# Kernel tuning notes

Hardware: AMD Instinct MI355X
Metric: run time of the kernel (lower is better)

The kernel has to match this reference:

```python
import jax, jax.numpy as jnp
import numpy as np
from jax import lax

B, C, H, W = 32, 128, 56, 56
SIZE = C * H * W
EPS = 1e-5
SLOPE = 0.1


def setup_inputs() -> dict:
    key = jax.random.key(0)
    ks = jax.random.split(key, 12)
    return {
        "ax": jax.random.normal(ks[0], (B, C, H, W), dtype=jnp.float32),
        "mx": jax.random.normal(ks[1], (B, C, H, W), dtype=jnp.float32),
        # grouped conv1d (groups=SIZE, k=2, no bias) == per-position pair weights [SIZE, 2]
        "cfc_w": jax.random.normal(ks[2], (SIZE, 2), dtype=jnp.float32) * 0.1,
        # BatchNorm1d (eval mode) params over SIZE channels
        "bn_gamma": jax.random.normal(ks[3], (SIZE,), dtype=jnp.float32) * 0.1 + 1.0,
        "bn_beta": jax.random.normal(ks[4], (SIZE,), dtype=jnp.float32) * 0.1,
        "bn_mean": jax.random.normal(ks[5], (SIZE,), dtype=jnp.float32) * 0.1,
        "bn_var": jax.random.uniform(ks[6], (SIZE,), dtype=jnp.float32, minval=0.5, maxval=1.5),
        # conv3x3, C->C, bias
        "conv_w": jax.random.normal(ks[7], (C, C, 3, 3), dtype=jnp.float32) * (1.0 / np.sqrt(C * 9)),
        "conv_b": jax.random.normal(ks[8], (C,), dtype=jnp.float32) * 0.01,
        # BatchNorm2d (eval mode) params over C channels
        "bn2_gamma": jax.random.normal(ks[9], (C,), dtype=jnp.float32) * 0.1 + 1.0,
        "bn2_beta": jax.random.normal(ks[10], (C,), dtype=jnp.float32) * 0.1,
        "bn2_mean": jax.random.normal(ks[11], (C,), dtype=jnp.float32) * 0.1,
        "bn2_var": jax.random.uniform(jax.random.fold_in(key, 99), (C,), dtype=jnp.float32, minval=0.5, maxval=1.5),
    }


def reference(ax, mx, cfc_w, bn_gamma, bn_beta, bn_mean, bn_var,
              conv_w, conv_b, bn2_gamma, bn2_beta, bn2_mean, bn2_var):
    b, c, h, w = ax.shape
    a = ax.reshape(b, -1)  # [B, SIZE]
    m = mx.reshape(b, -1)
    # degenerate grouped Conv1d(k=2, groups=SIZE): z_i = w_i0 * a_i + w_i1 * m_i
    z = cfc_w[:, 0] * a + cfc_w[:, 1] * m
    # BatchNorm1d (eval) + LeakyReLU(0.1)
    z = (z - bn_mean) * (bn_gamma / jnp.sqrt(bn_var + EPS)) + bn_beta
    z = jax.nn.leaky_relu(z, SLOPE).reshape(b, c, h, w)
    # conv3x3 (stride 1, pad 1) + bias
    y = lax.conv_general_dilated(z, conv_w, window_strides=(1, 1),
                                 padding=((1, 1), (1, 1)),
                                 dimension_numbers=("NCHW", "OIHW", "NCHW"))
    y = y + conv_b[None, :, None, None]
    # BatchNorm2d (eval) + LeakyReLU(0.1)
    scale = (bn2_gamma / jnp.sqrt(bn2_var + EPS))[None, :, None, None]
    y = (y - bn2_mean[None, :, None, None]) * scale + bn2_beta[None, :, None, None]
    return jax.nn.leaky_relu(y, SLOPE)
```

## Files before the change

kernel.cpp:

```cpp
#include <hip/hip_runtime.h>

#define B_ 32
#define C_ 128
#define H_ 56
#define W_ 56
#define HW_ (H_*W_)
#define SIZE_ (C_*HW_)
#define NPIX_ (B_*HW_)
#define HP_ 58
#define WP_ 58
#define PLANE_ (HP_*WP_*C_)
#define K_ 1152
#define EPS_ 1e-5f
#define SLOPE_ 0.1f

typedef __bf16 bf16x8 __attribute__((ext_vector_type(8)));
typedef float  f32x4  __attribute__((ext_vector_type(4)));

__device__ __forceinline__ ushort f2bf(float x) {
    union { float f; unsigned u; } v; v.f = x;
    return (ushort)((v.u + 0x7FFFu + ((v.u >> 16) & 1u)) >> 16);
}
__device__ __forceinline__ float lrelu(float z) { return z > 0.f ? z : SLOPE_ * z; }

__device__ __forceinline__ void glds16(const ushort* g, ushort* l) {
    __builtin_amdgcn_global_load_lds(
        (const __attribute__((address_space(1))) unsigned int*)g,
        (__attribute__((address_space(3))) unsigned int*)l, 16, 0, 0);
}

__global__ __launch_bounds__(256) void prep_kernel(
    const float* __restrict__ conv_w, const float* __restrict__ conv_b,
    const float* __restrict__ g2, const float* __restrict__ b2,
    const float* __restrict__ m2, const float* __restrict__ v2,
    const float2* __restrict__ cfc, const float* __restrict__ g1,
    const float* __restrict__ b1, const float* __restrict__ mu1,
    const float* __restrict__ v1,
    ushort* __restrict__ wA, float* __restrict__ scale2, float* __restrict__ shift2,
    float* __restrict__ p0, float* __restrict__ p1, float* __restrict__ p2)
{
    int tid = blockIdx.x * 256 + threadIdx.x;
    if (tid < C_ * K_) {
        int co = tid / K_;
        int k  = tid - co * K_;
        int khkw = k >> 7, ci = k & 127;
        int kh = khkw / 3, kw = khkw - 3 * kh;
        wA[tid] = f2bf(conv_w[((co * C_ + ci) * 3 + kh) * 3 + kw]);
    }
    if (tid < C_) {
        float sc = g2[tid] * rsqrtf(v2[tid] + EPS_);
        scale2[tid] = sc;
        shift2[tid] = (conv_b[tid] - m2[tid]) * sc + b2[tid];
    }
    if (tid < SIZE_) {
        float sc = g1[tid] * rsqrtf(v1[tid] + EPS_);
        float2 wv = cfc[tid];
        p0[tid] = wv.x * sc;
        p1[tid] = wv.y * sc;
        p2[tid] = b1[tid] - mu1[tid] * sc;
    }
}

__global__ __launch_bounds__(256) void zfuse_kernel(
    const float4* __restrict__ ax, const float4* __restrict__ mx,
    const float4* __restrict__ p0, const float4* __restrict__ p1,
    const float4* __restrict__ p2, ushort* __restrict__ zp)
{
    __shared__ ushort tile[W_ * 132];
    const int hp = blockIdx.x, b = blockIdx.y;
    const int tid = threadIdx.x;
    ushort* row = zp + (size_t)b * PLANE_ + (size_t)hp * (WP_ * C_);
    if (hp == 0 || hp == HP_ - 1) {
        uint2* r2 = (uint2*)row;
        for (int i = tid; i < WP_ * C_ / 4; i += 256) r2[i] = make_uint2(0u, 0u);
        return;
    }
    const int h = hp - 1;
    const int base4 = (b * SIZE_) >> 2;
    for (int i = tid; i < 1792; i += 256) {
        int c  = i / 14;
        int w4 = i - c * 14;
        int s4 = c * (HW_ / 4) + h * (W_ / 4) + w4;
        float4 a = ax[base4 + s4];
        float4 m = mx[base4 + s4];
        float4 q0 = p0[s4], q1 = p1[s4], q2 = p2[s4];
        int wb = w4 * 4;
        tile[(wb + 0) * 132 + c] = f2bf(lrelu(a.x * q0.x + m.x * q1.x + q2.x));
        tile[(wb + 1) * 132 + c] = f2bf(lrelu(a.y * q0.y + m.y * q1.y + q2.y));
        tile[(wb + 2) * 132 + c] = f2bf(lrelu(a.z * q0.z + m.z * q1.z + q2.z));
        tile[(wb + 3) * 132 + c] = f2bf(lrelu(a.w * q0.w + m.w * q1.w + q2.w));
    }
    __syncthreads();
    if (tid < C_) {
        row[tid] = 0;
        row[(WP_ - 1) * C_ + tid] = 0;
    }
    for (int j = tid; j < 1792; j += 256) {
        int w = j >> 5, cc = j & 31;
        *(uint2*)(row + C_ + w * C_ + cc * 4) = *(const uint2*)(tile + w * 132 + cc * 4);
    }
}

__global__ __launch_bounds__(256) void conv_kernel(
    const ushort* __restrict__ zp, const ushort* __restrict__ wA,
    const float* __restrict__ scale2, const float* __restrict__ shift2,
    float* __restrict__ out)
{
    __shared__ ushort As[2][128 * 32];
    __shared__ ushort Bs[2][128 * 32];

    const int tid  = threadIdx.x;
    const int wave = tid >> 6, lane = tid & 63;
    const int l16  = lane & 15, quad = lane >> 4;
    const int pbase = blockIdx.x * 128;

    const int srow = wave * 32 + (lane >> 2);
    const int skey = (srow >> 1) & 3;
    const int sch  = (lane & 3) ^ skey;
    const ushort* agA = wA + srow * K_ + sch * 8;

    int pf0 = pbase + srow;
    int bb0 = pf0 / HW_, pi0 = pf0 - bb0 * HW_;
    int h0 = pi0 / W_, w0 = pi0 - h0 * W_;
    const ushort* bgB0 = zp + (size_t)bb0 * PLANE_ + (h0 * WP_ + w0) * C_ + sch * 8;
    int pf1 = pf0 + 16;
    int bb1 = pf1 / HW_, pi1 = pf1 - bb1 * HW_;
    int h1 = pi1 / W_, w1 = pi1 - h1 * W_;
    const ushort* bgB1 = zp + (size_t)bb1 * PLANE_ + (h1 * WP_ + w1) * C_ + sch * 8;

    const int lofs0 = (wave * 32) * 32;
    const int lofs1 = (wave * 32 + 16) * 32;

    const int cob = (wave & 1) * 64;
    const int pxb = (wave >> 1) * 64;
    const int rquad = quad ^ ((l16 >> 1) & 3);

    f32x4 acc[4][4] = {};

#define STAGE(buf, aoff, boff)                                    \
    do {                                                          \
        glds16(agA + (aoff),           As[buf] + lofs0);          \
        glds16(agA + 16 * K_ + (aoff), As[buf] + lofs1);          \
        glds16(bgB0 + (boff),          Bs[buf] + lofs0);          \
        glds16(bgB1 + (boff),          Bs[buf] + lofs1);          \
    } while (0)

    STAGE(0, 0, 0);
    __syncthreads();

    int zoff = 0, kw = 0;
    for (int tap = 0; tap < 9; ++tap) {
        const int znext = (kw == 2) ? zoff + (WP_ - 2) * C_ : zoff + C_;
        #pragma unroll
        for (int ks = 0; ks < 4; ++ks) {
            const int buf  = ks & 1;
            const int step = tap * 4 + ks;
            if (step < 35) {
                const int boffn = (ks < 3) ? zoff + (ks + 1) * 32 : znext;
                STAGE(buf ^ 1, (step + 1) * 32, boffn);
            }
            bf16x8 af[4], bfr[4];
            #pragma unroll
            for (int mt = 0; mt < 4; ++mt)
                af[mt] = *(const bf16x8*)(As[buf] + (cob + mt * 16 + l16) * 32 + rquad * 8);
            #pragma unroll
            for (int nt = 0; nt < 4; ++nt)
                bfr[nt] = *(const bf16x8*)(Bs[buf] + (pxb + nt * 16 + l16) * 32 + rquad * 8);
            #pragma unroll
            for (int mt = 0; mt < 4; ++mt)
                #pragma unroll
                for (int nt = 0; nt < 4; ++nt)
                    acc[mt][nt] = __builtin_amdgcn_mfma_f32_16x16x32_bf16(
                        af[mt], bfr[nt], acc[mt][nt], 0, 0, 0);
            __syncthreads();
        }
        zoff = znext;
        if (kw == 2) kw = 0; else ++kw;
    }
#undef STAGE

    int pob[4];
    #pragma unroll
    for (int nt = 0; nt < 4; ++nt) {
        int pf = pbase + pxb + nt * 16 + l16;
        int bb = pf / HW_;
        pob[nt] = bb * SIZE_ + (pf - bb * HW_);
    }
    #pragma unroll
    for (int mt = 0; mt < 4; ++mt) {
        #pragma unroll
        for (int r = 0; r < 4; ++r) {
            int co = cob + mt * 16 + quad * 4 + r;
            float sc = scale2[co], sh = shift2[co];
            #pragma unroll
            for (int nt = 0; nt < 4; ++nt) {
                float v = acc[mt][nt][r] * sc + sh;
                out[(size_t)pob[nt] + co * HW_] = lrelu(v);
            }
        }
    }
}

extern "C" void kernel_launch(void* const* d_in, const int* in_sizes, int n_in,
                              void* d_out, int out_size, void* d_ws, size_t ws_size,
                              hipStream_t stream) {
    const float* ax     = (const float*)d_in[0];
    const float* mx     = (const float*)d_in[1];
    const float* cfc    = (const float*)d_in[2];
    const float* bn_g   = (const float*)d_in[3];
    const float* bn_b   = (const float*)d_in[4];
    const float* bn_m   = (const float*)d_in[5];
    const float* bn_v   = (const float*)d_in[6];
    const float* conv_w = (const float*)d_in[7];
    const float* conv_b = (const float*)d_in[8];
    const float* g2     = (const float*)d_in[9];
    const float* b2     = (const float*)d_in[10];
    const float* m2     = (const float*)d_in[11];
    const float* v2     = (const float*)d_in[12];
    float* out = (float*)d_out;

    char* ws = (char*)d_ws;
    ushort* zp     = (ushort*)ws;
    ushort* wA     = (ushort*)(ws + 27557888);
    float*  scale2 = (float*)(ws + 27852800);
    float*  shift2 = (float*)(ws + 27853312);
    float*  p0     = (float*)(ws + 27853824);
    float*  p1     = (float*)(ws + 29459456);
    float*  p2     = (float*)(ws + 31065088);

    prep_kernel<<<dim3((SIZE_ + 255) / 256), 256, 0, stream>>>(
        conv_w, conv_b, g2, b2, m2, v2, (const float2*)cfc,
        bn_g, bn_b, bn_m, bn_v, wA, scale2, shift2, p0, p1, p2);
    zfuse_kernel<<<dim3(HP_, B_), 256, 0, stream>>>(
        (const float4*)ax, (const float4*)mx,
        (const float4*)p0, (const float4*)p1, (const float4*)p2, zp);
    conv_kernel<<<dim3(NPIX_ / 128), 256, 0, stream>>>(zp, wA, scale2, shift2, out);
}
```

Before: 237.3 us.

## Triple-buffer conv K-loop with explicit vmcnt waits and single barrier

Replaces the double-buffered LDS pipeline in the conv GEMM with a three-stage ring. Loads are issued two steps ahead, and the wait uses s_waitcnt vmcnt(4) plus one barrier per step instead of a full sync after the MFMAs. The 36-step loop is fully unrolled with compile-time B offsets, and launch bounds now ask for 3 blocks per CU. The goal is to hide global-to-LDS latency behind MFMA work, at the cost of 50% more LDS and a tighter register budget.

New measurement: 241.8 us. Within noise of the previous version (+1.9%).

```diff
diff --git a/kernel.cpp b/kernel.cpp
--- a/kernel.cpp
+++ b/kernel.cpp
@@ -101,13 +101,13 @@
     }
 }
 
-__global__ __launch_bounds__(256) void conv_kernel(
+__global__ __launch_bounds__(256, 3) void conv_kernel(
     const ushort* __restrict__ zp, const ushort* __restrict__ wA,
     const float* __restrict__ scale2, const float* __restrict__ shift2,
     float* __restrict__ out)
 {
-    __shared__ ushort As[2][128 * 32];
-    __shared__ ushort Bs[2][128 * 32];
+    __shared__ ushort As[3][128 * 32];
+    __shared__ ushort Bs[3][128 * 32];
 
     const int tid  = threadIdx.x;
     const int wave = tid >> 6, lane = tid & 63;
@@ -145,39 +145,38 @@
         glds16(bgB1 + (boff),          Bs[buf] + lofs1);          \
     } while (0)
 
-    STAGE(0, 0, 0);
-    __syncthreads();
-
-    int zoff = 0, kw = 0;
-    for (int tap = 0; tap < 9; ++tap) {
-        const int znext = (kw == 2) ? zoff + (WP_ - 2) * C_ : zoff + C_;
-        #pragma unroll
-        for (int ks = 0; ks < 4; ++ks) {
-            const int buf  = ks & 1;
-            const int step = tap * 4 + ks;
-            if (step < 35) {
-                const int boffn = (ks < 3) ? zoff + (ks + 1) * 32 : znext;
-                STAGE(buf ^ 1, (step + 1) * 32, boffn);
-            }
-            bf16x8 af[4], bfr[4];
-            #pragma unroll
-            for (int mt = 0; mt < 4; ++mt)
-                af[mt] = *(const bf16x8*)(As[buf] + (cob + mt * 16 + l16) * 32 + rquad * 8);
+#define BOFF(t) ((((t) >> 2) / 3 * WP_ + ((t) >> 2) % 3) * C_ + ((t) & 3) * 32)
+
+    STAGE(0, 0, BOFF(0));
+    STAGE(1, 32, BOFF(1));
+
+    #pragma unroll
+    for (int t = 0; t < 36; ++t) {
+        if (t < 35) asm volatile("s_waitcnt vmcnt(4)" ::: "memory");
+        else        asm volatile("s_waitcnt vmcnt(0)" ::: "memory");
+        __builtin_amdgcn_s_barrier();
+        __builtin_amdgcn_sched_barrier(0);
+        if (t <= 33) {
+            const int t2 = t + 2;
+            STAGE(t2 % 3, t2 * 32, BOFF(t2));
+        }
+        const int buf = t % 3;
+        bf16x8 af[4], bfr[4];
+        #pragma unroll
+        for (int mt = 0; mt < 4; ++mt)
+            af[mt] = *(const bf16x8*)(As[buf] + (cob + mt * 16 + l16) * 32 + rquad * 8);
+        #pragma unroll
+        for (int nt = 0; nt < 4; ++nt)
+            bfr[nt] = *(const bf16x8*)(Bs[buf] + (pxb + nt * 16 + l16) * 32 + rquad * 8);
+        #pragma unroll
+        for (int mt = 0; mt < 4; ++mt)
             #pragma unroll
             for (int nt = 0; nt < 4; ++nt)
-                bfr[nt] = *(const bf16x8*)(Bs[buf] + (pxb + nt * 16 + l16) * 32 + rquad * 8);
-            #pragma unroll
-            for (int mt = 0; mt < 4; ++mt)
-                #pragma unroll
-                for (int nt = 0; nt < 4; ++nt)
-                    acc[mt][nt] = __builtin_amdgcn_mfma_f32_16x16x32_bf16(
-                        af[mt], bfr[nt], acc[mt][nt], 0, 0, 0);
-            __syncthreads();
-        }
-        zoff = znext;
-        if (kw == 2) kw = 0; else ++kw;
+                acc[mt][nt] = __builtin_amdgcn_mfma_f32_16x16x32_bf16(
+                    af[mt], bfr[nt], acc[mt][nt], 0, 0, 0);
     }
 #undef STAGE
+#undef BOFF
 
     int pob[4];
     #pragma unroll
```
